# Optimization experiments

Measured on AMD Instinct MI355X. Metric: run time of the kernel, lower is better.

Reference implementation:

```python
import jax, jax.numpy as jnp
import numpy as np

E = 8            # moe_num_experts
FFN = 8192       # ffn_hidden_size
D = 2048         # d_model
B, T = 1, 4096


def setup_inputs() -> dict:
    key = jax.random.key(0)
    k1, k2, k3, k4 = jax.random.split(key, 4)
    x = jax.random.normal(k1, (B, T, D), dtype=jnp.float32)
    # params stored flat as (E*FFN, D), as in the flax module
    w1 = jax.random.normal(k2, (E * FFN, D), dtype=jnp.float32) * 0.02
    v1 = jax.random.normal(k3, (E * FFN, D), dtype=jnp.float32) * 0.02
    w2 = jax.random.normal(k4, (E * FFN, D), dtype=jnp.float32) * 0.02
    return {"x": x, "w1": w1, "v1": v1, "w2": w2, "expert_idx": 3}


def reference(x, w1, v1, w2, expert_idx):
    # select this expert's weight slabs: (FFN, D) each
    expert_shape = (E, FFN, D)
    ew1 = w1.reshape(expert_shape)[expert_idx]
    ev1 = v1.reshape(expert_shape)[expert_idx]
    ew2 = w2.reshape(expert_shape)[expert_idx]
    # gate and up projections: [B,T,D] x [D,FFN] -> [B,T,FFN]
    x1 = jnp.einsum('btd,fd->btf', x, ew1)
    x2 = jnp.einsum('btd,fd->btf', x, ev1)
    h = jax.nn.silu(x1) * x2
    # down projection (note: matmul with ew2, i.e. contraction over FFN)
    out = jnp.einsum('btf,fd->btd', h, ew2)
    return out
```

## Files before the change

kernel.cpp:

```cpp
#include <hip/hip_runtime.h>

#define E_NUM 8
#define FFN_DIM 8192
#define D_DIM 2048
#define T_DIM 4096

using bf16x8 = __attribute__((ext_vector_type(8))) short;
using f32x4  = __attribute__((ext_vector_type(4))) float;
using u16x8  = __attribute__((ext_vector_type(8))) unsigned short;

__device__ __forceinline__ unsigned short f2bf(float f) {
  union { float f; unsigned int u; } v; v.f = f;
  unsigned int u = v.u;
  unsigned int r = (u + 0x7FFFu + ((u >> 16) & 1u)) >> 16;
  return (unsigned short)r;
}

__device__ __forceinline__ void gload16(const unsigned short* g, const unsigned short* l) {
  __builtin_amdgcn_global_load_lds(
      (const __attribute__((address_space(1))) void*)g,
      (__attribute__((address_space(3))) void*)l, 16, 0, 0);
}

__global__ void convert_kernel(const float* __restrict__ src_base,
                               const int* __restrict__ eidx, long slab,
                               unsigned short* __restrict__ dst, long n) {
  const float* src = src_base + (long)(*eidx) * slab;
  long stride = (long)gridDim.x * blockDim.x;
  for (long i = (long)blockIdx.x * blockDim.x + threadIdx.x; i * 8 < n; i += stride) {
    long e = i * 8;
    const float4* p = (const float4*)(src + e);
    float4 f0 = p[0], f1 = p[1];
    u16x8 o;
    o[0] = f2bf(f0.x); o[1] = f2bf(f0.y); o[2] = f2bf(f0.z); o[3] = f2bf(f0.w);
    o[4] = f2bf(f1.x); o[5] = f2bf(f1.y); o[6] = f2bf(f1.z); o[7] = f2bf(f1.w);
    *(u16x8*)(dst + e) = o;
  }
}

__global__ void transpose_kernel(const float* __restrict__ w2,
                                 const int* __restrict__ eidx,
                                 unsigned short* __restrict__ dst) {
  __shared__ unsigned short tile[32][33];
  const float* src = w2 + (long)(*eidx) * (long)FFN_DIM * D_DIM;
  int d0 = blockIdx.x << 5;
  int f0 = blockIdx.y << 5;
  int tx = threadIdx.x & 31, ty = threadIdx.x >> 5;
#pragma unroll
  for (int i = 0; i < 4; ++i) {
    int f = ty + i * 8;
    tile[f][tx] = f2bf(src[(long)(f0 + f) * D_DIM + d0 + tx]);
  }
  __syncthreads();
#pragma unroll
  for (int i = 0; i < 4; ++i) {
    int d = ty + i * 8;
    dst[(long)(d0 + d) * FFN_DIM + f0 + tx] = tile[tx][d];
  }
}

#define VMCNT8 asm volatile("s_waitcnt vmcnt(8)" ::: "memory")
#define VMCNT6 asm volatile("s_waitcnt vmcnt(6)" ::: "memory")
#define VMCNT0 asm volatile("s_waitcnt vmcnt(0)" ::: "memory")
#define BAR __builtin_amdgcn_s_barrier()
#define PRIO1 __builtin_amdgcn_s_setprio(1)
#define PRIO0 __builtin_amdgcn_s_setprio(0)

__global__ __launch_bounds__(512, 2) void gemm1_silu(
    const unsigned short* __restrict__ Xb,
    const unsigned short* __restrict__ W1b,
    const unsigned short* __restrict__ V1b,
    unsigned short* __restrict__ Hb) {
  __shared__ __align__(16) unsigned short sA[2 * 2 * 8192];
  __shared__ __align__(16) unsigned short sB1[2 * 8192];
  __shared__ __align__(16) unsigned short sB2[2 * 8192];

  const int tid = threadIdx.x;
  const int wv = tid >> 6, l = tid & 63;
  const int wm = wv >> 2, wn = wv & 3;
  const int kq = l >> 4, lr = l & 15;
  const int bsw = (blockIdx.x & 7) * 128 + (blockIdx.x >> 3);
  const int m0 = (bsw & 15) << 8;
  const int n0 = (bsw >> 4) << 7;

  const int rsub = tid >> 3;
  const int sslot8 = ((tid & 7) ^ ((tid >> 3) & 7)) << 3;
  const unsigned short* gA  = Xb  + (long)(m0 + rsub) * D_DIM + sslot8;
  const unsigned short* gB1 = W1b + (long)(n0 + rsub) * D_DIM + sslot8;
  const unsigned short* gB2 = V1b + (long)(n0 + rsub) * D_DIM + sslot8;

#define STG(gbase, rowoff, tc_, lbase) do { \
    gload16((gbase) + (long)(rowoff) * D_DIM + (tc_), (lbase) + wv * 512); \
    gload16((gbase) + (long)((rowoff) + 64) * D_DIM + (tc_), (lbase) + 4096 + wv * 512); \
  } while (0)

  int aoff[4], boff[2];
#pragma unroll
  for (int j = 0; j < 4; ++j) {
    int row = wm * 64 + j * 16 + lr;
    aoff[j] = row * 64 + ((kq ^ (row & 7)) << 3);
  }
#pragma unroll
  for (int g = 0; g < 2; ++g) {
    int row = wn * 32 + g * 16 + lr;
    boff[g] = row * 64 + ((kq ^ (row & 7)) << 3);
  }

  f32x4 acc1[8][2], acc2[8][2];
  f32x4 z = {0.f, 0.f, 0.f, 0.f};
#pragma unroll
  for (int f = 0; f < 8; ++f)
#pragma unroll
    for (int g = 0; g < 2; ++g) { acc1[f][g] = z; acc2[f][g] = z; }

  STG(gA, 0, 0, sA);
  STG(gA, 128, 0, sA + 8192);
  STG(gB1, 0, 0, sB1);
  STG(gB2, 0, 0, sB2);
  STG(gA, 0, 64, sA + 16384);
  STG(gA, 128, 64, sA + 24576);
  STG(gB1, 0, 64, sB1 + 8192);
  STG(gB2, 0, 64, sB2 + 8192);
  VMCNT8;
  BAR;

  const int NT = D_DIM / 64;
  for (int t = 0; t < NT; ++t) {
    const int db = t & 1;
    const unsigned short* A0p = sA + (db * 2 + 0) * 8192;
    const unsigned short* A1p = sA + (db * 2 + 1) * 8192;
    const unsigned short* B1p = sB1 + db * 8192;
    const unsigned short* B2p = sB2 + db * 8192;
    const int p1ok = (t + 1 < NT), p2ok = (t + 2 < NT);
    const int tc2 = (t + 2) << 6;
    bf16x8 aA[4][2], aB[4][2], b1[2][2], b2[2][2];

#pragma unroll
    for (int j = 0; j < 4; ++j) {
      aA[j][0] = *(const bf16x8*)(A0p + aoff[j]);
      aA[j][1] = *(const bf16x8*)(A0p + (aoff[j] ^ 32));
    }
#pragma unroll
    for (int g = 0; g < 2; ++g) {
      b1[g][0] = *(const bf16x8*)(B1p + boff[g]);
      b1[g][1] = *(const bf16x8*)(B1p + (boff[g] ^ 32));
    }
    BAR;
    PRIO1;
#pragma unroll
    for (int j = 0; j < 4; ++j)
#pragma unroll
      for (int g = 0; g < 2; ++g) {
        acc1[j][g] = __builtin_amdgcn_mfma_f32_16x16x32_bf16(aA[j][0], b1[g][0], acc1[j][g], 0, 0, 0);
        acc1[j][g] = __builtin_amdgcn_mfma_f32_16x16x32_bf16(aA[j][1], b1[g][1], acc1[j][g], 0, 0, 0);
      }
    PRIO0;
    BAR;

#pragma unroll
    for (int j = 0; j < 4; ++j) {
      aB[j][0] = *(const bf16x8*)(A1p + aoff[j]);
      aB[j][1] = *(const bf16x8*)(A1p + (aoff[j] ^ 32));
    }
    if (p2ok) {
      STG(gA, 0, tc2, sA + (db * 2 + 0) * 8192);
      STG(gB1, 0, tc2, sB1 + db * 8192);
    }
    BAR;
    PRIO1;
#pragma unroll
    for (int j = 0; j < 4; ++j)
#pragma unroll
      for (int g = 0; g < 2; ++g) {
        acc1[4 + j][g] = __builtin_amdgcn_mfma_f32_16x16x32_bf16(aB[j][0], b1[g][0], acc1[4 + j][g], 0, 0, 0);
        acc1[4 + j][g] = __builtin_amdgcn_mfma_f32_16x16x32_bf16(aB[j][1], b1[g][1], acc1[4 + j][g], 0, 0, 0);
      }
    PRIO0;
    BAR;

#pragma unroll
    for (int g = 0; g < 2; ++g) {
      b2[g][0] = *(const bf16x8*)(B2p + boff[g]);
      b2[g][1] = *(const bf16x8*)(B2p + (boff[g] ^ 32));
    }
    if (p2ok) STG(gA, 128, tc2, sA + (db * 2 + 1) * 8192);
    BAR;
    PRIO1;
#pragma unroll
    for (int j = 0; j < 4; ++j)
#pragma unroll
      for (int g = 0; g < 2; ++g) {
        acc2[j][g] = __builtin_amdgcn_mfma_f32_16x16x32_bf16(aA[j][0], b2[g][0], acc2[j][g], 0, 0, 0);
        acc2[j][g] = __builtin_amdgcn_mfma_f32_16x16x32_bf16(aA[j][1], b2[g][1], acc2[j][g], 0, 0, 0);
      }
    PRIO0;
    BAR;

    if (p2ok) STG(gB2, 0, tc2, sB2 + db * 8192);
    BAR;
    PRIO1;
#pragma unroll
    for (int j = 0; j < 4; ++j)
#pragma unroll
      for (int g = 0; g < 2; ++g) {
        acc2[4 + j][g] = __builtin_amdgcn_mfma_f32_16x16x32_bf16(aB[j][0], b2[g][0], acc2[4 + j][g], 0, 0, 0);
        acc2[4 + j][g] = __builtin_amdgcn_mfma_f32_16x16x32_bf16(aB[j][1], b2[g][1], acc2[4 + j][g], 0, 0, 0);
      }
    PRIO0;
    if (p2ok) { VMCNT8; } else if (p1ok) { VMCNT0; }
    BAR;
  }

#pragma unroll
  for (int f = 0; f < 8; ++f)
#pragma unroll
    for (int g = 0; g < 2; ++g)
#pragma unroll
      for (int r = 0; r < 4; ++r) {
        int row = m0 + (f >> 2) * 128 + wm * 64 + (f & 3) * 16 + kq * 4 + r;
        int col = n0 + wn * 32 + g * 16 + lr;
        float x1 = acc1[f][g][r], x2 = acc2[f][g][r];
        float hv = x1 / (1.f + __expf(-x1)) * x2;
        Hb[(long)row * FFN_DIM + col] = f2bf(hv);
      }
#undef STG
}

__global__ __launch_bounds__(512, 2) void gemm2(
    const unsigned short* __restrict__ Hb,
    const unsigned short* __restrict__ W2T,
    float* __restrict__ out) {
  __shared__ __align__(16) unsigned short sA[2 * 2 * 8192];
  __shared__ __align__(16) unsigned short sB[2 * 8192];

  const int tid = threadIdx.x;
  const int wv = tid >> 6, l = tid & 63;
  const int wm = wv >> 1, wn = wv & 1;
  const int kq = l >> 4, lr = l & 15;
  const int bsw = (blockIdx.x & 7) * 32 + (blockIdx.x >> 3);
  const int m0 = (bsw & 15) << 8;
  const int n0 = (bsw >> 4) << 7;
  const int hA = wm >> 1;

  const int rsub = tid >> 3;
  const int sslot8 = ((tid & 7) ^ ((tid >> 3) & 7)) << 3;
  const unsigned short* gA = Hb  + (long)(m0 + rsub) * FFN_DIM + sslot8;
  const unsigned short* gB = W2T + (long)(n0 + rsub) * FFN_DIM + sslot8;

#define STG2(gbase, rowoff, tc_, lbase) do { \
    gload16((gbase) + (long)(rowoff) * FFN_DIM + (tc_), (lbase) + wv * 512); \
    gload16((gbase) + (long)((rowoff) + 64) * FFN_DIM + (tc_), (lbase) + 4096 + wv * 512); \
  } while (0)

  int aoff[4], boff[4];
#pragma unroll
  for (int f = 0; f < 4; ++f) {
    int row = (wm & 1) * 64 + f * 16 + lr;
    aoff[f] = row * 64 + ((kq ^ (row & 7)) << 3);
  }
#pragma unroll
  for (int g = 0; g < 4; ++g) {
    int row = wn * 64 + g * 16 + lr;
    boff[g] = row * 64 + ((kq ^ (row & 7)) << 3);
  }

  f32x4 acc[4][4];
  f32x4 z = {0.f, 0.f, 0.f, 0.f};
#pragma unroll
  for (int f = 0; f < 4; ++f)
#pragma unroll
    for (int g = 0; g < 4; ++g) acc[f][g] = z;

  STG2(gA, 0, 0, sA);
  STG2(gA, 128, 0, sA + 8192);
  STG2(gB, 0, 0, sB);
  STG2(gA, 0, 64, sA + 16384);
  STG2(gA, 128, 64, sA + 24576);
  STG2(gB, 0, 64, sB + 8192);
  VMCNT6;
  BAR;

  const int NT = FFN_DIM / 64;
  for (int t = 0; t < NT; ++t) {
    const int db = t & 1;
    const unsigned short* Ap = sA + (db * 2 + hA) * 8192;
    const unsigned short* Bp = sB + db * 8192;
    const int p1ok = (t + 1 < NT), p2ok = (t + 2 < NT);
    const int tc2 = (t + 2) << 6;
    bf16x8 aA[2][2], aB[2][2], bA[2][2], bB[2][2];

#pragma unroll
    for (int f = 0; f < 2; ++f) {
      aA[f][0] = *(const bf16x8*)(Ap + aoff[f]);
      aA[f][1] = *(const bf16x8*)(Ap + (aoff[f] ^ 32));
    }
#pragma unroll
    for (int g = 0; g < 2; ++g) {
      bA[g][0] = *(const bf16x8*)(Bp + boff[g]);
      bA[g][1] = *(const bf16x8*)(Bp + (boff[g] ^ 32));
    }
    BAR;
    PRIO1;
#pragma unroll
    for (int f = 0; f < 2; ++f)
#pragma unroll
      for (int g = 0; g < 2; ++g) {
        acc[f][g] = __builtin_amdgcn_mfma_f32_16x16x32_bf16(aA[f][0], bA[g][0], acc[f][g], 0, 0, 0);
        acc[f][g] = __builtin_amdgcn_mfma_f32_16x16x32_bf16(aA[f][1], bA[g][1], acc[f][g], 0, 0, 0);
      }
    PRIO0;
    BAR;

#pragma unroll
    for (int f = 0; f < 2; ++f) {
      aB[f][0] = *(const bf16x8*)(Ap + aoff[2 + f]);
      aB[f][1] = *(const bf16x8*)(Ap + (aoff[2 + f] ^ 32));
    }
    BAR;
    PRIO1;
#pragma unroll
    for (int f = 0; f < 2; ++f)
#pragma unroll
      for (int g = 0; g < 2; ++g) {
        acc[2 + f][g] = __builtin_amdgcn_mfma_f32_16x16x32_bf16(aB[f][0], bA[g][0], acc[2 + f][g], 0, 0, 0);
        acc[2 + f][g] = __builtin_amdgcn_mfma_f32_16x16x32_bf16(aB[f][1], bA[g][1], acc[2 + f][g], 0, 0, 0);
      }
    PRIO0;
    BAR;

#pragma unroll
    for (int g = 0; g < 2; ++g) {
      bB[g][0] = *(const bf16x8*)(Bp + boff[2 + g]);
      bB[g][1] = *(const bf16x8*)(Bp + (boff[2 + g] ^ 32));
    }
    if (p2ok) {
      STG2(gA, 0, tc2, sA + (db * 2 + 0) * 8192);
      STG2(gA, 128, tc2, sA + (db * 2 + 1) * 8192);
    }
    BAR;
    PRIO1;
#pragma unroll
    for (int f = 0; f < 2; ++f)
#pragma unroll
      for (int g = 0; g < 2; ++g) {
        acc[f][2 + g] = __builtin_amdgcn_mfma_f32_16x16x32_bf16(aA[f][0], bB[g][0], acc[f][2 + g], 0, 0, 0);
        acc[f][2 + g] = __builtin_amdgcn_mfma_f32_16x16x32_bf16(aA[f][1], bB[g][1], acc[f][2 + g], 0, 0, 0);
      }
    PRIO0;
    BAR;

    if (p2ok) STG2(gB, 0, tc2, sB + db * 8192);
    BAR;
    PRIO1;
#pragma unroll
    for (int f = 0; f < 2; ++f)
#pragma unroll
      for (int g = 0; g < 2; ++g) {
        acc[2 + f][2 + g] = __builtin_amdgcn_mfma_f32_16x16x32_bf16(aB[f][0], bB[g][0], acc[2 + f][2 + g], 0, 0, 0);
        acc[2 + f][2 + g] = __builtin_amdgcn_mfma_f32_16x16x32_bf16(aB[f][1], bB[g][1], acc[2 + f][2 + g], 0, 0, 0);
      }
    PRIO0;
    if (p2ok) { VMCNT6; } else if (p1ok) { VMCNT0; }
    BAR;
  }

#pragma unroll
  for (int f = 0; f < 4; ++f)
#pragma unroll
    for (int g = 0; g < 4; ++g)
#pragma unroll
      for (int r = 0; r < 4; ++r) {
        int row = m0 + wm * 64 + f * 16 + kq * 4 + r;
        int col = n0 + wn * 64 + g * 16 + lr;
        out[(long)row * D_DIM + col] = acc[f][g][r];
      }
#undef STG2
}

extern "C" void kernel_launch(void* const* d_in, const int* in_sizes, int n_in,
                              void* d_out, int out_size, void* d_ws, size_t ws_size,
                              hipStream_t stream) {
  const float* x  = (const float*)d_in[0];
  const float* w1 = (const float*)d_in[1];
  const float* v1 = (const float*)d_in[2];
  const float* w2 = (const float*)d_in[3];
  const int* eidx = (const int*)d_in[4];

  char* ws = (char*)d_ws;
  unsigned short* Xb  = (unsigned short*)(ws);
  unsigned short* W1b = (unsigned short*)(ws + (16l << 20));
  unsigned short* V1b = (unsigned short*)(ws + (48l << 20));
  unsigned short* W2T = (unsigned short*)(ws + (80l << 20));
  unsigned short* Hb  = (unsigned short*)(ws + (112l << 20));
  float* out = (float*)d_out;

  long slab = (long)FFN_DIM * D_DIM;
  transpose_kernel<<<dim3(D_DIM / 32, FFN_DIM / 32), 256, 0, stream>>>(w2, eidx, W2T);
  convert_kernel<<<2048, 256, 0, stream>>>(w1, eidx, slab, W1b, slab);
  convert_kernel<<<2048, 256, 0, stream>>>(v1, eidx, slab, V1b, slab);
  convert_kernel<<<2048, 256, 0, stream>>>(x,  eidx, 0,    Xb,  (long)T_DIM * D_DIM);
  gemm1_silu<<<1024, 512, 0, stream>>>(Xb, W1b, V1b, Hb);
  gemm2<<<256, 512, 0, stream>>>(Hb, W2T, out);
}
```

Baseline: 490.6 us.

## Restructure GEMM pipelines to prefetch LDS fragments across iterations with fewer barriers

Both GEMM kernels now load the next K-tile's register fragments from LDS during the current tile's MFMA phases and split global-to-LDS staging into finer chunks spread over the phases. This cuts the barrier count per iteration from six or eight down to four. The block-to-tile mapping is flipped so that consecutive blocks share M rows instead of N columns. The transpose kernel moves to 64x64 tiles with float4 reads and 16-byte writes. The tighter vmcnt accounting and explicit lgkmcnt waits in the barrier macro add correctness risk around buffer reuse.

Result: no change. 486.5 us (-0.8%).

```diff
diff --git a/kernel.cpp b/kernel.cpp
--- a/kernel.cpp
+++ b/kernel.cpp
@@ -38,31 +38,37 @@
   }
 }
 
-__global__ void transpose_kernel(const float* __restrict__ w2,
-                                 const int* __restrict__ eidx,
-                                 unsigned short* __restrict__ dst) {
-  __shared__ unsigned short tile[32][33];
+__global__ __launch_bounds__(512) void transpose_kernel(
+    const float* __restrict__ w2, const int* __restrict__ eidx,
+    unsigned short* __restrict__ dst) {
+  __shared__ unsigned short tile[64][72];
   const float* src = w2 + (long)(*eidx) * (long)FFN_DIM * D_DIM;
-  int d0 = blockIdx.x << 5;
-  int f0 = blockIdx.y << 5;
-  int tx = threadIdx.x & 31, ty = threadIdx.x >> 5;
-#pragma unroll
-  for (int i = 0; i < 4; ++i) {
-    int f = ty + i * 8;
-    tile[f][tx] = f2bf(src[(long)(f0 + f) * D_DIM + d0 + tx]);
+  const int tid = threadIdx.x;
+  int d0 = blockIdx.x << 6;
+  int f0 = blockIdx.y << 6;
+#pragma unroll
+  for (int p = 0; p < 2; ++p) {
+    int f = p * 32 + (tid >> 4);
+    int dc = (tid & 15) * 4;
+    float4 v = *(const float4*)(src + (long)(f0 + f) * D_DIM + d0 + dc);
+    tile[f][dc + 0] = f2bf(v.x); tile[f][dc + 1] = f2bf(v.y);
+    tile[f][dc + 2] = f2bf(v.z); tile[f][dc + 3] = f2bf(v.w);
   }
   __syncthreads();
-#pragma unroll
-  for (int i = 0; i < 4; ++i) {
-    int d = ty + i * 8;
-    dst[(long)(d0 + d) * FFN_DIM + f0 + tx] = tile[tx][d];
-  }
+  int d = tid >> 3;
+  int fc = (tid & 7) * 8;
+  u16x8 o;
+#pragma unroll
+  for (int j = 0; j < 8; ++j) o[j] = tile[fc + j][d];
+  *(u16x8*)(dst + (long)(d0 + d) * FFN_DIM + f0 + fc) = o;
 }
 
 #define VMCNT8 asm volatile("s_waitcnt vmcnt(8)" ::: "memory")
 #define VMCNT6 asm volatile("s_waitcnt vmcnt(6)" ::: "memory")
+#define VMCNT5 asm volatile("s_waitcnt vmcnt(5)" ::: "memory")
+#define VMCNT3 asm volatile("s_waitcnt vmcnt(3)" ::: "memory")
 #define VMCNT0 asm volatile("s_waitcnt vmcnt(0)" ::: "memory")
-#define BAR __builtin_amdgcn_s_barrier()
+#define BAR asm volatile("s_waitcnt lgkmcnt(0)\n\ts_barrier" ::: "memory")
 #define PRIO1 __builtin_amdgcn_s_setprio(1)
 #define PRIO0 __builtin_amdgcn_s_setprio(0)
 
@@ -71,7 +77,7 @@
     const unsigned short* __restrict__ W1b,
     const unsigned short* __restrict__ V1b,
     unsigned short* __restrict__ Hb) {
-  __shared__ __align__(16) unsigned short sA[2 * 2 * 8192];
+  __shared__ __align__(16) unsigned short sA[2 * 16384];
   __shared__ __align__(16) unsigned short sB1[2 * 8192];
   __shared__ __align__(16) unsigned short sB2[2 * 8192];
 
@@ -80,8 +86,8 @@
   const int wm = wv >> 2, wn = wv & 3;
   const int kq = l >> 4, lr = l & 15;
   const int bsw = (blockIdx.x & 7) * 128 + (blockIdx.x >> 3);
-  const int m0 = (bsw & 15) << 8;
-  const int n0 = (bsw >> 4) << 7;
+  const int m0 = (bsw >> 6) << 8;
+  const int n0 = (bsw & 63) << 7;
 
   const int rsub = tid >> 3;
   const int sslot8 = ((tid & 7) ^ ((tid >> 3) & 7)) << 3;
@@ -89,16 +95,16 @@
   const unsigned short* gB1 = W1b + (long)(n0 + rsub) * D_DIM + sslot8;
   const unsigned short* gB2 = V1b + (long)(n0 + rsub) * D_DIM + sslot8;
 
-#define STG(gbase, rowoff, tc_, lbase) do { \
-    gload16((gbase) + (long)(rowoff) * D_DIM + (tc_), (lbase) + wv * 512); \
-    gload16((gbase) + (long)((rowoff) + 64) * D_DIM + (tc_), (lbase) + 4096 + wv * 512); \
-  } while (0)
-
-  int aoff[4], boff[2];
+#define STG1(gbase, r_, tc_, lbase) \
+  gload16((gbase) + (long)((r_) * 64) * D_DIM + (tc_), (lbase) + (r_) * 4096 + wv * 512)
+
+  int aoffA[4], aoffB[4], boff[2];
 #pragma unroll
   for (int j = 0; j < 4; ++j) {
-    int row = wm * 64 + j * 16 + lr;
-    aoff[j] = row * 64 + ((kq ^ (row & 7)) << 3);
+    int rowA = wm * 64 + j * 16 + lr;
+    aoffA[j] = rowA * 64 + ((kq ^ (rowA & 7)) << 3);
+    int rowB = 128 + wm * 64 + j * 16 + lr;
+    aoffB[j] = rowB * 64 + ((kq ^ (rowB & 7)) << 3);
   }
 #pragma unroll
   for (int g = 0; g < 2; ++g) {
@@ -113,39 +119,48 @@
 #pragma unroll
     for (int g = 0; g < 2; ++g) { acc1[f][g] = z; acc2[f][g] = z; }
 
-  STG(gA, 0, 0, sA);
-  STG(gA, 128, 0, sA + 8192);
-  STG(gB1, 0, 0, sB1);
-  STG(gB2, 0, 0, sB2);
-  STG(gA, 0, 64, sA + 16384);
-  STG(gA, 128, 64, sA + 24576);
-  STG(gB1, 0, 64, sB1 + 8192);
-  STG(gB2, 0, 64, sB2 + 8192);
+  bf16x8 aA[4][2], aB[4][2], b1[2][2], b2[2][2];
+
+  STG1(gB1, 0, 0, sB1); STG1(gB1, 1, 0, sB1);
+  STG1(gA, 0, 0, sA); STG1(gA, 1, 0, sA); STG1(gA, 2, 0, sA); STG1(gA, 3, 0, sA);
+  STG1(gB2, 0, 0, sB2); STG1(gB2, 1, 0, sB2);
+  STG1(gB1, 0, 64, sB1 + 8192); STG1(gB1, 1, 64, sB1 + 8192);
+  STG1(gA, 0, 64, sA + 16384); STG1(gA, 1, 64, sA + 16384);
+  STG1(gA, 2, 64, sA + 16384); STG1(gA, 3, 64, sA + 16384);
+  STG1(gB2, 0, 64, sB2 + 8192); STG1(gB2, 1, 64, sB2 + 8192);
   VMCNT8;
   BAR;
+#pragma unroll
+  for (int j = 0; j < 4; ++j) {
+    aA[j][0] = *(const bf16x8*)(sA + aoffA[j]);
+    aA[j][1] = *(const bf16x8*)(sA + (aoffA[j] ^ 32));
+  }
+#pragma unroll
+  for (int g = 0; g < 2; ++g) {
+    b1[g][0] = *(const bf16x8*)(sB1 + boff[g]);
+    b1[g][1] = *(const bf16x8*)(sB1 + (boff[g] ^ 32));
+  }
+  BAR;
 
   const int NT = D_DIM / 64;
   for (int t = 0; t < NT; ++t) {
-    const int db = t & 1;
-    const unsigned short* A0p = sA + (db * 2 + 0) * 8192;
-    const unsigned short* A1p = sA + (db * 2 + 1) * 8192;
-    const unsigned short* B1p = sB1 + db * 8192;
-    const unsigned short* B2p = sB2 + db * 8192;
+    const int db = t & 1, nx = db ^ 1;
+    const unsigned short* Acur  = sA  + db * 16384;
+    const unsigned short* Anxt  = sA  + nx * 16384;
+    const unsigned short* B1nxt = sB1 + nx * 8192;
+    const unsigned short* B2cur = sB2 + db * 8192;
+    unsigned short* AcurW  = (unsigned short*)sA  + db * 16384;
+    unsigned short* B1curW = (unsigned short*)sB1 + db * 8192;
+    unsigned short* B2curW = (unsigned short*)sB2 + db * 8192;
     const int p1ok = (t + 1 < NT), p2ok = (t + 2 < NT);
     const int tc2 = (t + 2) << 6;
-    bf16x8 aA[4][2], aB[4][2], b1[2][2], b2[2][2];
 
 #pragma unroll
     for (int j = 0; j < 4; ++j) {
-      aA[j][0] = *(const bf16x8*)(A0p + aoff[j]);
-      aA[j][1] = *(const bf16x8*)(A0p + (aoff[j] ^ 32));
-    }
-#pragma unroll
-    for (int g = 0; g < 2; ++g) {
-      b1[g][0] = *(const bf16x8*)(B1p + boff[g]);
-      b1[g][1] = *(const bf16x8*)(B1p + (boff[g] ^ 32));
-    }
-    BAR;
+      aB[j][0] = *(const bf16x8*)(Acur + aoffB[j]);
+      aB[j][1] = *(const bf16x8*)(Acur + (aoffB[j] ^ 32));
+    }
+    if (p2ok) { STG1(gB1, 0, tc2, B1curW); STG1(gB1, 1, tc2, B1curW); }
     PRIO1;
 #pragma unroll
     for (int j = 0; j < 4; ++j)
@@ -158,15 +173,11 @@
     BAR;
 
 #pragma unroll
-    for (int j = 0; j < 4; ++j) {
-      aB[j][0] = *(const bf16x8*)(A1p + aoff[j]);
-      aB[j][1] = *(const bf16x8*)(A1p + (aoff[j] ^ 32));
-    }
-    if (p2ok) {
-      STG(gA, 0, tc2, sA + (db * 2 + 0) * 8192);
-      STG(gB1, 0, tc2, sB1 + db * 8192);
-    }
-    BAR;
+    for (int g = 0; g < 2; ++g) {
+      b2[g][0] = *(const bf16x8*)(B2cur + boff[g]);
+      b2[g][1] = *(const bf16x8*)(B2cur + (boff[g] ^ 32));
+    }
+    if (p2ok) { STG1(gA, 0, tc2, AcurW); STG1(gA, 1, tc2, AcurW); STG1(gA, 2, tc2, AcurW); }
     PRIO1;
 #pragma unroll
     for (int j = 0; j < 4; ++j)
@@ -176,15 +187,10 @@
         acc1[4 + j][g] = __builtin_amdgcn_mfma_f32_16x16x32_bf16(aB[j][1], b1[g][1], acc1[4 + j][g], 0, 0, 0);
       }
     PRIO0;
-    BAR;
-
-#pragma unroll
-    for (int g = 0; g < 2; ++g) {
-      b2[g][0] = *(const bf16x8*)(B2p + boff[g]);
-      b2[g][1] = *(const bf16x8*)(B2p + (boff[g] ^ 32));
-    }
-    if (p2ok) STG(gA, 128, tc2, sA + (db * 2 + 1) * 8192);
-    BAR;
+    if (p2ok) { VMCNT5; } else if (p1ok) { VMCNT0; }
+    BAR;
+
+    if (p2ok) { STG1(gA, 3, tc2, AcurW); STG1(gB2, 0, tc2, B2curW); STG1(gB2, 1, tc2, B2curW); }
     PRIO1;
 #pragma unroll
     for (int j = 0; j < 4; ++j)
@@ -194,10 +200,15 @@
         acc2[j][g] = __builtin_amdgcn_mfma_f32_16x16x32_bf16(aA[j][1], b2[g][1], acc2[j][g], 0, 0, 0);
       }
     PRIO0;
-    BAR;
-
-    if (p2ok) STG(gB2, 0, tc2, sB2 + db * 8192);
-    BAR;
+    if (p1ok) {
+#pragma unroll
+      for (int j = 0; j < 4; ++j) {
+        aA[j][0] = *(const bf16x8*)(Anxt + aoffA[j]);
+        aA[j][1] = *(const bf16x8*)(Anxt + (aoffA[j] ^ 32));
+      }
+    }
+    BAR;
+
     PRIO1;
 #pragma unroll
     for (int j = 0; j < 4; ++j)
@@ -207,7 +218,13 @@
         acc2[4 + j][g] = __builtin_amdgcn_mfma_f32_16x16x32_bf16(aB[j][1], b2[g][1], acc2[4 + j][g], 0, 0, 0);
       }
     PRIO0;
-    if (p2ok) { VMCNT8; } else if (p1ok) { VMCNT0; }
+    if (p1ok) {
+#pragma unroll
+      for (int g = 0; g < 2; ++g) {
+        b1[g][0] = *(const bf16x8*)(B1nxt + boff[g]);
+        b1[g][1] = *(const bf16x8*)(B1nxt + (boff[g] ^ 32));
+      }
+    }
     BAR;
   }
 
@@ -223,14 +240,14 @@
         float hv = x1 / (1.f + __expf(-x1)) * x2;
         Hb[(long)row * FFN_DIM + col] = f2bf(hv);
       }
-#undef STG
+#undef STG1
 }
 
 __global__ __launch_bounds__(512, 2) void gemm2(
     const unsigned short* __restrict__ Hb,
     const unsigned short* __restrict__ W2T,
     float* __restrict__ out) {
-  __shared__ __align__(16) unsigned short sA[2 * 2 * 8192];
+  __shared__ __align__(16) unsigned short sA[2 * 16384];
   __shared__ __align__(16) unsigned short sB[2 * 8192];
 
   const int tid = threadIdx.x;
@@ -238,24 +255,21 @@
   const int wm = wv >> 1, wn = wv & 1;
   const int kq = l >> 4, lr = l & 15;
   const int bsw = (blockIdx.x & 7) * 32 + (blockIdx.x >> 3);
-  const int m0 = (bsw & 15) << 8;
-  const int n0 = (bsw >> 4) << 7;
-  const int hA = wm >> 1;
+  const int m0 = (bsw >> 4) << 8;
+  const int n0 = (bsw & 15) << 7;
 
   const int rsub = tid >> 3;
   const int sslot8 = ((tid & 7) ^ ((tid >> 3) & 7)) << 3;
   const unsigned short* gA = Hb  + (long)(m0 + rsub) * FFN_DIM + sslot8;
   const unsigned short* gB = W2T + (long)(n0 + rsub) * FFN_DIM + sslot8;
 
-#define STG2(gbase, rowoff, tc_, lbase) do { \
-    gload16((gbase) + (long)(rowoff) * FFN_DIM + (tc_), (lbase) + wv * 512); \
-    gload16((gbase) + (long)((rowoff) + 64) * FFN_DIM + (tc_), (lbase) + 4096 + wv * 512); \
-  } while (0)
+#define STG1(gbase, r_, tc_, lbase) \
+  gload16((gbase) + (long)((r_) * 64) * FFN_DIM + (tc_), (lbase) + (r_) * 4096 + wv * 512)
 
   int aoff[4], boff[4];
 #pragma unroll
   for (int f = 0; f < 4; ++f) {
-    int row = (wm & 1) * 64 + f * 16 + lr;
+    int row = wm * 64 + f * 16 + lr;
     aoff[f] = row * 64 + ((kq ^ (row & 7)) << 3);
   }
 #pragma unroll
@@ -271,35 +285,49 @@
 #pragma unroll
     for (int g = 0; g < 4; ++g) acc[f][g] = z;
 
-  STG2(gA, 0, 0, sA);
-  STG2(gA, 128, 0, sA + 8192);
-  STG2(gB, 0, 0, sB);
-  STG2(gA, 0, 64, sA + 16384);
-  STG2(gA, 128, 64, sA + 24576);
-  STG2(gB, 0, 64, sB + 8192);
+  bf16x8 aA[2][2], aB[2][2], bA[2][2], bB[2][2];
+
+  STG1(gB, 0, 0, sB); STG1(gB, 1, 0, sB);
+  STG1(gA, 0, 0, sA); STG1(gA, 1, 0, sA); STG1(gA, 2, 0, sA); STG1(gA, 3, 0, sA);
+  STG1(gB, 0, 64, sB + 8192); STG1(gB, 1, 64, sB + 8192);
+  STG1(gA, 0, 64, sA + 16384); STG1(gA, 1, 64, sA + 16384);
+  STG1(gA, 2, 64, sA + 16384); STG1(gA, 3, 64, sA + 16384);
   VMCNT6;
   BAR;
+#pragma unroll
+  for (int f = 0; f < 2; ++f) {
+    aA[f][0] = *(const bf16x8*)(sA + aoff[f]);
+    aA[f][1] = *(const bf16x8*)(sA + (aoff[f] ^ 32));
+  }
+#pragma unroll
+  for (int g = 0; g < 2; ++g) {
+    bA[g][0] = *(const bf16x8*)(sB + boff[g]);
+    bA[g][1] = *(const bf16x8*)(sB + (boff[g] ^ 32));
+  }
+  BAR;
 
   const int NT = FFN_DIM / 64;
   for (int t = 0; t < NT; ++t) {
-    const int db = t & 1;
-    const unsigned short* Ap = sA + (db * 2 + hA) * 8192;
-    const unsigned short* Bp = sB + db * 8192;
+    const int db = t & 1, nx = db ^ 1;
+    const unsigned short* Acur = sA + db * 16384;
+    const unsigned short* Anxt = sA + nx * 16384;
+    const unsigned short* Bcur = sB + db * 8192;
+    const unsigned short* Bnxt = sB + nx * 8192;
+    unsigned short* AcurW = (unsigned short*)sA + db * 16384;
+    unsigned short* BcurW = (unsigned short*)sB + db * 8192;
     const int p1ok = (t + 1 < NT), p2ok = (t + 2 < NT);
     const int tc2 = (t + 2) << 6;
-    bf16x8 aA[2][2], aB[2][2], bA[2][2], bB[2][2];
 
 #pragma unroll
     for (int f = 0; f < 2; ++f) {
-      aA[f][0] = *(const bf16x8*)(Ap + aoff[f]);
-      aA[f][1] = *(const bf16x8*)(Ap + (aoff[f] ^ 32));
+      aB[f][0] = *(const bf16x8*)(Acur + aoff[2 + f]);
+      aB[f][1] = *(const bf16x8*)(Acur + (aoff[2 + f] ^ 32));
     }
 #pragma unroll
     for (int g = 0; g < 2; ++g) {
-      bA[g][0] = *(const bf16x8*)(Bp + boff[g]);
-      bA[g][1] = *(const bf16x8*)(Bp + (boff[g] ^ 32));
-    }
-    BAR;
+      bB[g][0] = *(const bf16x8*)(Bcur + boff[2 + g]);
+      bB[g][1] = *(const bf16x8*)(Bcur + (boff[2 + g] ^ 32));
+    }
     PRIO1;
 #pragma unroll
     for (int f = 0; f < 2; ++f)
@@ -311,12 +339,7 @@
     PRIO0;
     BAR;
 
-#pragma unroll
-    for (int f = 0; f < 2; ++f) {
-      aB[f][0] = *(const bf16x8*)(Ap + aoff[2 + f]);
-      aB[f][1] = *(const bf16x8*)(Ap + (aoff[2 + f] ^ 32));
-    }
-    BAR;
+    if (p2ok) { STG1(gB, 0, tc2, BcurW); STG1(gB, 1, tc2, BcurW); STG1(gA, 0, tc2, AcurW); }
     PRIO1;
 #pragma unroll
     for (int f = 0; f < 2; ++f)
@@ -326,18 +349,10 @@
         acc[2 + f][g] = __builtin_amdgcn_mfma_f32_16x16x32_bf16(aB[f][1], bA[g][1], acc[2 + f][g], 0, 0, 0);
       }
     PRIO0;
-    BAR;
-
-#pragma unroll
-    for (int g = 0; g < 2; ++g) {
-      bB[g][0] = *(const bf16x8*)(Bp + boff[2 + g]);
-      bB[g][1] = *(const bf16x8*)(Bp + (boff[2 + g] ^ 32));
-    }
-    if (p2ok) {
-      STG2(gA, 0, tc2, sA + (db * 2 + 0) * 8192);
-      STG2(gA, 128, tc2, sA + (db * 2 + 1) * 8192);
-    }
-    BAR;
+    if (p2ok) { VMCNT3; } else if (p1ok) { VMCNT0; }
+    BAR;
+
+    if (p2ok) { STG1(gA, 1, tc2, AcurW); STG1(gA, 2, tc2, AcurW); STG1(gA, 3, tc2, AcurW); }
     PRIO1;
 #pragma unroll
     for (int f = 0; f < 2; ++f)
@@ -347,10 +362,15 @@
         acc[f][2 + g] = __builtin_amdgcn_mfma_f32_16x16x32_bf16(aA[f][1], bB[g][1], acc[f][2 + g], 0, 0, 0);
       }
     PRIO0;
-    BAR;
-
-    if (p2ok) STG2(gB, 0, tc2, sB + db * 8192);
-    BAR;
+    if (p1ok) {
+#pragma unroll
+      for (int f = 0; f < 2; ++f) {
+        aA[f][0] = *(const bf16x8*)(Anxt + aoff[f]);
+        aA[f][1] = *(const bf16x8*)(Anxt + (aoff[f] ^ 32));
+      }
+    }
+    BAR;
+
     PRIO1;
 #pragma unroll
     for (int f = 0; f < 2; ++f)
@@ -360,7 +380,13 @@
         acc[2 + f][2 + g] = __builtin_amdgcn_mfma_f32_16x16x32_bf16(aB[f][1], bB[g][1], acc[2 + f][2 + g], 0, 0, 0);
       }
     PRIO0;
-    if (p2ok) { VMCNT6; } else if (p1ok) { VMCNT0; }
+    if (p1ok) {
+#pragma unroll
+      for (int g = 0; g < 2; ++g) {
+        bA[g][0] = *(const bf16x8*)(Bnxt + boff[g]);
+        bA[g][1] = *(const bf16x8*)(Bnxt + (boff[g] ^ 32));
+      }
+    }
     BAR;
   }
 
@@ -374,7 +400,7 @@
         int col = n0 + wn * 64 + g * 16 + lr;
         out[(long)row * D_DIM + col] = acc[f][g][r];
       }
-#undef STG2
+#undef STG1
 }
 
 extern "C" void kernel_launch(void* const* d_in, const int* in_sizes, int n_in,
@@ -395,7 +421,7 @@
   float* out = (float*)d_out;
 
   long slab = (long)FFN_DIM * D_DIM;
-  transpose_kernel<<<dim3(D_DIM / 32, FFN_DIM / 32), 256, 0, stream>>>(w2, eidx, W2T);
+  transpose_kernel<<<dim3(D_DIM / 64, FFN_DIM / 64), 512, 0, stream>>>(w2, eidx, W2T);
   convert_kernel<<<2048, 256, 0, stream>>>(w1, eidx, slab, W1b, slab);
   convert_kernel<<<2048, 256, 0, stream>>>(v1, eidx, slab, V1b, slab);
   convert_kernel<<<2048, 256, 0, stream>>>(x,  eidx, 0,    Xb,  (long)T_DIM * D_DIM);
```
